# Kernel tuning notes

Hardware: AMD Instinct MI355X
Metric: run time of the kernel (lower is better)

The kernel has to match this reference:

```python
import jax, jax.numpy as jnp
import numpy as np

N, E, IN_DIM, OUT_DIM, HEADS = 50000, 800000, 128, 64, 2
NEG_SLOPE = 0.2  # DGL GATConv default leaky_relu slope


def setup_inputs() -> dict:
    key = jax.random.key(0)
    ks = jax.random.split(key, 11)
    p = lambda k, shape: jax.random.normal(k, shape, jnp.float32) * 0.05
    return dict(
        feature=jax.random.normal(ks[0], (N, IN_DIM), jnp.float32),
        src=jax.random.randint(ks[1], (E,), 0, N, jnp.int32),
        dst=jax.random.randint(ks[2], (E,), 0, N, jnp.int32),
        W1=p(ks[3], (IN_DIM, HEADS * OUT_DIM)),
        al1=p(ks[4], (HEADS, OUT_DIM)),
        ar1=p(ks[5], (HEADS, OUT_DIM)),
        b1=p(ks[6], (HEADS * OUT_DIM,)),
        W2=p(ks[7], (HEADS * OUT_DIM, OUT_DIM)),
        al2=p(ks[8], (1, OUT_DIM)),
        ar2=p(ks[9], (1, OUT_DIM)),
        b2=p(ks[10], (OUT_DIM,)),
    )


def gat_conv(x, W, al, ar, b, src, dst, n_nodes):
    # DGL GATConv (eval mode): fc -> per-node attn halves -> edge leaky_relu
    # -> edge-softmax grouped by dst -> scatter-weighted sum -> + bias
    H, D = al.shape
    h = (x @ W).reshape(n_nodes, H, D)               # [N,H,D]
    el = jnp.einsum('nhd,hd->nh', h, al)             # [N,H]
    er = jnp.einsum('nhd,hd->nh', h, ar)             # [N,H]
    e = jax.nn.leaky_relu(el[src] + er[dst], NEG_SLOPE)  # [E,H]
    m = jax.ops.segment_max(e, dst, num_segments=n_nodes)
    m = jnp.where(jnp.isfinite(m), m, 0.0)           # guard isolated dst nodes
    ex = jnp.exp(e - m[dst])                         # [E,H]
    s = jax.ops.segment_sum(ex, dst, num_segments=n_nodes)
    alpha = ex / s[dst]                              # edge-softmax weights
    out = jax.ops.segment_sum(alpha[:, :, None] * h[src], dst,
                              num_segments=n_nodes)  # [N,H,D]
    return out + b.reshape(H, D)


def reference(feature, src, dst, W1, al1, ar1, b1, W2, al2, ar2, b2):
    h1 = jax.nn.elu(gat_conv(feature, W1, al1, ar1, b1, src, dst, N))  # [N,2,D]
    h2 = gat_conv(h1.reshape(N, -1), W2, al2, ar2, b2, src, dst, N)    # [N,1,D]
    return (h1.mean(axis=1) + h2[:, 0, :]) * 0.5
```

## Files before the change

kernel.cpp:

```cpp
#include <hip/hip_runtime.h>
#include <hip/hip_fp16.h>
#include <math.h>

#define NNODES 50000
#define NEDGES 800000
#define CSR_STRIDE 48

typedef short bf16x8 __attribute__((ext_vector_type(8)));
typedef float f32x4  __attribute__((ext_vector_type(4)));

__device__ __forceinline__ unsigned bfpack(float a, float b) {
    unsigned ua = __float_as_uint(a), ub = __float_as_uint(b);
    ua = (ua + 0x7fffu + ((ua >> 16) & 1u)) >> 16;
    ub = (ub + 0x7fffu + ((ub >> 16) & 1u)) >> 16;
    return ua | (ub << 16);
}
__device__ __forceinline__ unsigned h2pack(float a, float b) {
    __half2 h = __floats2half2_rn(a, b);
    return *(unsigned*)&h;
}
__device__ __forceinline__ float hlo(unsigned u) {
    union { unsigned u; __half2 h; } c; c.u = u; return __half2float(c.h.x);
}
__device__ __forceinline__ float hhi(unsigned u) {
    union { unsigned u; __half2 h; } c; c.u = u; return __half2float(c.h.y);
}

__global__ __launch_bounds__(256) void fill_fused_kernel(
    const int* __restrict__ src, const int* __restrict__ dst,
    int* __restrict__ deg, unsigned short* __restrict__ pcsr) {
    const int t  = blockIdx.x * 256 + threadIdx.x;
    const int e0 = t * 4;
    if (e0 + 3 < NEDGES) {
        int4 d4 = *(const int4*)&dst[e0];
        int4 s4 = *(const int4*)&src[e0];
        int p0 = atomicAdd(&deg[d4.x], 1);
        int p1 = atomicAdd(&deg[d4.y], 1);
        int p2 = atomicAdd(&deg[d4.z], 1);
        int p3 = atomicAdd(&deg[d4.w], 1);
        if (p0 < CSR_STRIDE) pcsr[d4.x * CSR_STRIDE + p0] = (unsigned short)s4.x;
        if (p1 < CSR_STRIDE) pcsr[d4.y * CSR_STRIDE + p1] = (unsigned short)s4.y;
        if (p2 < CSR_STRIDE) pcsr[d4.z * CSR_STRIDE + p2] = (unsigned short)s4.z;
        if (p3 < CSR_STRIDE) pcsr[d4.w * CSR_STRIDE + p3] = (unsigned short)s4.w;
    } else if (e0 < NEDGES) {
        for (int e = e0; e < NEDGES; ++e) {
            int d = dst[e], s = src[e];
            int p = atomicAdd(&deg[d], 1);
            if (p < CSR_STRIDE) pcsr[d * CSR_STRIDE + p] = (unsigned short)s;
        }
    }
}

__global__ __launch_bounds__(256) void wt_kernel(const float* __restrict__ W1,
                                                 const float* __restrict__ W2,
                                                 unsigned* __restrict__ W1t,
                                                 unsigned* __restrict__ W2t) {
    int w = blockIdx.x * 256 + threadIdx.x;
    if (w < 8192) {
        int n = w >> 6, j = w & 63;
        W1t[w] = bfpack(W1[(2 * j) * 128 + n], W1[(2 * j + 1) * 128 + n]);
    } else {
        int w2 = w - 8192;
        int n = w2 >> 6, j = w2 & 63;
        W2t[w2] = bfpack(W2[(2 * j) * 64 + n], W2[(2 * j + 1) * 64 + n]);
    }
}

__global__ __launch_bounds__(256) void gemm1_kernel(
    const float* __restrict__ feat, const unsigned* __restrict__ Wt,
    const float* __restrict__ al, const float* __restrict__ ar,
    unsigned* __restrict__ h, float* __restrict__ el, float* __restrict__ er) {
    __shared__ unsigned Wb[128 * 68];
    __shared__ unsigned Ab[64 * 68];
    const int tid = threadIdx.x;
    const int n0  = blockIdx.x * 64;

#pragma unroll
    for (int i = 0; i < 8; ++i) {
        int id = i * 256 + tid;
        int n = id >> 4, c = (id & 15) * 4;
        *(uint4*)&Wb[n * 68 + c] = *(const uint4*)&Wt[n * 64 + c];
    }
#pragma unroll
    for (int i = 0; i < 8; ++i) {
        int f = i * 256 + tid;
        int m = f >> 5, cf = (f & 31) * 4;
        float4 v = make_float4(0.f, 0.f, 0.f, 0.f);
        if (n0 + m < NNODES)
            v = *(const float4*)&feat[(size_t)(n0 + m) * 128 + cf];
        uint2 p = {bfpack(v.x, v.y), bfpack(v.z, v.w)};
        *(uint2*)&Ab[m * 68 + cf / 2] = p;
    }
    __syncthreads();

    const int w  = tid >> 6;
    const int l  = tid & 63;
    const int ml = l & 15;
    const int q  = l >> 4;
    f32x4 acc[8];
#pragma unroll
    for (int t = 0; t < 8; ++t) acc[t] = (f32x4){0.f, 0.f, 0.f, 0.f};

#pragma unroll
    for (int kc = 0; kc < 4; ++kc) {
        const int kw = kc * 16 + q * 4;
        uint4 a4 = *(uint4*)&Ab[(16 * w + ml) * 68 + kw];
        bf16x8 af = *(bf16x8*)&a4;
#pragma unroll
        for (int t = 0; t < 8; ++t) {
            uint4 b4 = *(uint4*)&Wb[(t * 16 + ml) * 68 + kw];
            bf16x8 bf = *(bf16x8*)&b4;
            acc[t] = __builtin_amdgcn_mfma_f32_16x16x32_bf16(af, bf, acc[t], 0, 0, 0);
        }
    }

    float av[8], rv[8];
#pragma unroll
    for (int t = 0; t < 8; ++t) { av[t] = al[t * 16 + ml]; rv[t] = ar[t * 16 + ml]; }

#pragma unroll
    for (int r = 0; r < 4; ++r) {
        const int node = n0 + 16 * w + q * 4 + r;
        float e0 = 0.f, e1 = 0.f, f0 = 0.f, f1 = 0.f;
#pragma unroll
        for (int t = 0; t < 8; ++t) {
            float v = acc[t][r];
            if (t < 4) { e0 = fmaf(v, av[t], e0); f0 = fmaf(v, rv[t], f0); }
            else       { e1 = fmaf(v, av[t], e1); f1 = fmaf(v, rv[t], f1); }
            float pv = __shfl_xor(v, 1);
            if ((ml & 1) == 0 && node < NNODES)
                h[(size_t)node * 64 + t * 8 + (ml >> 1)] = h2pack(v, pv);
        }
#pragma unroll
        for (int mm = 1; mm <= 8; mm <<= 1) {
            e0 += __shfl_xor(e0, mm); e1 += __shfl_xor(e1, mm);
            f0 += __shfl_xor(f0, mm); f1 += __shfl_xor(f1, mm);
        }
        if (ml == 0 && node < NNODES) {
            el[node * 2 + 0] = e0; el[node * 2 + 1] = e1;
            er[node * 2 + 0] = f0; er[node * 2 + 1] = f1;
        }
    }
}

__global__ __launch_bounds__(256) void gemm2_kernel(
    const unsigned* __restrict__ h1b, const unsigned* __restrict__ Wt,
    const float* __restrict__ al, const float* __restrict__ ar,
    unsigned* __restrict__ h2, float* __restrict__ el, float* __restrict__ er) {
    __shared__ unsigned Wb[64 * 68];
    __shared__ unsigned Ab[64 * 68];
    const int tid = threadIdx.x;
    const int n0  = blockIdx.x * 64;

#pragma unroll
    for (int i = 0; i < 4; ++i) {
        int id = i * 256 + tid;
        int n = id >> 4, c = (id & 15) * 4;
        *(uint4*)&Wb[n * 68 + c] = *(const uint4*)&Wt[n * 64 + c];
    }
#pragma unroll
    for (int i = 0; i < 4; ++i) {
        int id = i * 256 + tid;
        int m = id >> 4, c = (id & 15) * 4;
        uint4 v = make_uint4(0u, 0u, 0u, 0u);
        if (n0 + m < NNODES)
            v = *(const uint4*)&h1b[(size_t)(n0 + m) * 64 + c];
        *(uint4*)&Ab[m * 68 + c] = v;
    }
    __syncthreads();

    const int w  = tid >> 6;
    const int l  = tid & 63;
    const int ml = l & 15;
    const int q  = l >> 4;
    f32x4 acc[4];
#pragma unroll
    for (int t = 0; t < 4; ++t) acc[t] = (f32x4){0.f, 0.f, 0.f, 0.f};

#pragma unroll
    for (int kc = 0; kc < 4; ++kc) {
        const int kw = kc * 16 + q * 4;
        uint4 a4 = *(uint4*)&Ab[(16 * w + ml) * 68 + kw];
        bf16x8 af = *(bf16x8*)&a4;
#pragma unroll
        for (int t = 0; t < 4; ++t) {
            uint4 b4 = *(uint4*)&Wb[(t * 16 + ml) * 68 + kw];
            bf16x8 bf = *(bf16x8*)&b4;
            acc[t] = __builtin_amdgcn_mfma_f32_16x16x32_bf16(af, bf, acc[t], 0, 0, 0);
        }
    }

    float av[4], rv[4];
#pragma unroll
    for (int t = 0; t < 4; ++t) { av[t] = al[t * 16 + ml]; rv[t] = ar[t * 16 + ml]; }

#pragma unroll
    for (int r = 0; r < 4; ++r) {
        const int node = n0 + 16 * w + q * 4 + r;
        float e0 = 0.f, f0 = 0.f;
#pragma unroll
        for (int t = 0; t < 4; ++t) {
            float v = acc[t][r];
            e0 = fmaf(v, av[t], e0);
            f0 = fmaf(v, rv[t], f0);
            float pv = __shfl_xor(v, 1);
            if ((ml & 1) == 0 && node < NNODES)
                h2[(size_t)node * 32 + t * 8 + (ml >> 1)] = h2pack(v, pv);
        }
#pragma unroll
        for (int mm = 1; mm <= 8; mm <<= 1) {
            e0 += __shfl_xor(e0, mm);
            f0 += __shfl_xor(f0, mm);
        }
        if (ml == 0 && node < NNODES) { el[node] = e0; er[node] = f0; }
    }
}

#define FMA8(hv, A)                                              \
    a0r = fmaf(hlo(hv.x), A, a0r); a1r = fmaf(hhi(hv.x), A, a1r); \
    a2r = fmaf(hlo(hv.y), A, a2r); a3r = fmaf(hhi(hv.y), A, a3r); \
    a4r = fmaf(hlo(hv.z), A, a4r); a5r = fmaf(hhi(hv.z), A, a5r); \
    a6r = fmaf(hlo(hv.w), A, a6r); a7r = fmaf(hhi(hv.w), A, a7r);

__global__ __launch_bounds__(256) void aggregate1_kernel(
    const int* __restrict__ degv,
    const unsigned short* __restrict__ csr_src,
    const float* __restrict__ el, const float* __restrict__ er,
    const unsigned* __restrict__ hh, const float* __restrict__ bias,
    unsigned* __restrict__ h1b, float* __restrict__ hm) {
    const int wid  = (blockIdx.x * 256 + threadIdx.x) >> 6;
    const int lane = threadIdx.x & 63;
    const int hl   = lane & 31;
    const int lb   = lane & 32;
    const int node = wid * 2 + (lane >> 5);
    if (node >= NNODES) return;
    const int row = node * CSR_STRIDE;
    int deg = degv[node];
    deg = deg < CSR_STRIDE ? deg : CSR_STRIDE;
    const float er0 = er[node * 2 + 0];
    const float er1 = er[node * 2 + 1];

    const int  q2    = hl >> 4;
    const int  ql    = hl & 15;
    const bool h1sel = (ql >= 8);
    const unsigned* __restrict__ hq = hh + 4 * ql;

    int s_reg = 0;
    if (hl < deg) s_reg = (int)csr_src[row + hl];

    uint4 hv[8];
#pragma unroll
    for (int j = 0; j < 8; ++j) {
        int s = __shfl(s_reg, lb + 2 * j + q2);
        hv[j] = *(const uint4*)(hq + (size_t)s * 64);
    }
    int dm  = deg < 32 ? deg : 32;
    int dmW = max(dm, __shfl_xor(dm, 32));
    const bool doB = dmW > 16;
    uint4 hw[8];
    if (doB) {
#pragma unroll
        for (int j = 0; j < 8; ++j) {
            int s = __shfl(s_reg, lb + 16 + 2 * j + q2);
            hw[j] = *(const uint4*)(hq + (size_t)s * 64);
        }
    }

    float2 e2 = *(const float2*)&el[s_reg * 2];
    float a = e2.x + er0; a = a > 0.f ? a : 0.2f * a;
    float b = e2.y + er1; b = b > 0.f ? b : 0.2f * b;
    float v0 = (hl < deg) ? a : -1e30f;
    float v1 = (hl < deg) ? b : -1e30f;
    float m0 = v0, m1 = v1;
    for (int i = 32 + hl; i < deg; i += 32) {
        int s = (int)csr_src[row + i];
        float2 ee = *(const float2*)&el[s * 2];
        float aa = ee.x + er0; aa = aa > 0.f ? aa : 0.2f * aa;
        float bb = ee.y + er1; bb = bb > 0.f ? bb : 0.2f * bb;
        m0 = fmaxf(m0, aa); m1 = fmaxf(m1, bb);
    }
#pragma unroll
    for (int off = 16; off > 0; off >>= 1) {
        m0 = fmaxf(m0, __shfl_xor(m0, off));
        m1 = fmaxf(m1, __shfl_xor(m1, off));
    }
    float p0 = __expf(v0 - m0);
    float p1 = __expf(v1 - m1);
    float ssum0 = p0, ssum1 = p1;
    for (int i = 32 + hl; i < deg; i += 32) {
        int s = (int)csr_src[row + i];
        float2 ee = *(const float2*)&el[s * 2];
        float aa = ee.x + er0; aa = aa > 0.f ? aa : 0.2f * aa;
        float bb = ee.y + er1; bb = bb > 0.f ? bb : 0.2f * bb;
        ssum0 += __expf(aa - m0); ssum1 += __expf(bb - m1);
    }
#pragma unroll
    for (int off = 16; off > 0; off >>= 1) {
        ssum0 += __shfl_xor(ssum0, off);
        ssum1 += __shfl_xor(ssum1, off);
    }

    float a0r = 0.f, a1r = 0.f, a2r = 0.f, a3r = 0.f;
    float a4r = 0.f, a5r = 0.f, a6r = 0.f, a7r = 0.f;
#pragma unroll
    for (int j = 0; j < 8; ++j) {
        const int sl_ = lb + 2 * j + q2;
        float x = __shfl(p0, sl_);
        float y = __shfl(p1, sl_);
        float A = h1sel ? y : x;
        FMA8(hv[j], A)
    }
    if (doB) {
#pragma unroll
        for (int j = 0; j < 8; ++j) {
            const int sl_ = lb + 16 + 2 * j + q2;
            float x = __shfl(p0, sl_);
            float y = __shfl(p1, sl_);
            float A = h1sel ? y : x;
            FMA8(hw[j], A)
        }
    }
    for (int i2 = 32; i2 < deg; i2 += 2) {
        int eidx = i2 + q2;
        if (eidx < deg) {
            int s = (int)csr_src[row + eidx];
            float2 ee = *(const float2*)&el[s * 2];
            float aa = ee.x + er0; aa = aa > 0.f ? aa : 0.2f * aa;
            float bb = ee.y + er1; bb = bb > 0.f ? bb : 0.2f * bb;
            float alpha = h1sel ? __expf(bb - m1) : __expf(aa - m0);
            uint4 h4 = *(const uint4*)(hq + (size_t)s * 64);
            FMA8(h4, alpha)
        }
    }
    a0r += __shfl_xor(a0r, 16);  a1r += __shfl_xor(a1r, 16);
    a2r += __shfl_xor(a2r, 16);  a3r += __shfl_xor(a3r, 16);
    a4r += __shfl_xor(a4r, 16);  a5r += __shfl_xor(a5r, 16);
    a6r += __shfl_xor(a6r, 16);  a7r += __shfl_xor(a7r, 16);

    const float ssum = h1sel ? ssum1 : ssum0;
    const float inv  = (deg > 0) ? 1.f / ssum : 0.f;
    float4 b0 = *(const float4*)&bias[8 * ql];
    float4 b1 = *(const float4*)&bias[8 * ql + 4];
    float o0 = fmaf(a0r, inv, b0.x), o1 = fmaf(a1r, inv, b0.y);
    float o2 = fmaf(a2r, inv, b0.z), o3 = fmaf(a3r, inv, b0.w);
    float o4 = fmaf(a4r, inv, b1.x), o5 = fmaf(a5r, inv, b1.y);
    float o6 = fmaf(a6r, inv, b1.z), o7 = fmaf(a7r, inv, b1.w);
    o0 = o0 > 0.f ? o0 : (__expf(o0) - 1.f);
    o1 = o1 > 0.f ? o1 : (__expf(o1) - 1.f);
    o2 = o2 > 0.f ? o2 : (__expf(o2) - 1.f);
    o3 = o3 > 0.f ? o3 : (__expf(o3) - 1.f);
    o4 = o4 > 0.f ? o4 : (__expf(o4) - 1.f);
    o5 = o5 > 0.f ? o5 : (__expf(o5) - 1.f);
    o6 = o6 > 0.f ? o6 : (__expf(o6) - 1.f);
    o7 = o7 > 0.f ? o7 : (__expf(o7) - 1.f);

    if (hl < 16) {
        uint4 pk;
        pk.x = bfpack(o0, o1); pk.y = bfpack(o2, o3);
        pk.z = bfpack(o4, o5); pk.w = bfpack(o6, o7);
        *(uint4*)&h1b[(size_t)node * 64 + 4 * ql] = pk;
    }
    float n0_ = 0.5f * (o0 + __shfl_xor(o0, 8));
    float n1_ = 0.5f * (o1 + __shfl_xor(o1, 8));
    float n2_ = 0.5f * (o2 + __shfl_xor(o2, 8));
    float n3_ = 0.5f * (o3 + __shfl_xor(o3, 8));
    float n4_ = 0.5f * (o4 + __shfl_xor(o4, 8));
    float n5_ = 0.5f * (o5 + __shfl_xor(o5, 8));
    float n6_ = 0.5f * (o6 + __shfl_xor(o6, 8));
    float n7_ = 0.5f * (o7 + __shfl_xor(o7, 8));
    if (hl < 8) {
        *(float4*)&hm[(size_t)node * 64 + 8 * hl]     = make_float4(n0_, n1_, n2_, n3_);
        *(float4*)&hm[(size_t)node * 64 + 8 * hl + 4] = make_float4(n4_, n5_, n6_, n7_);
    }
}

#define FMA4(hv, P)                                            \
    ax = fmaf(hlo(hv.x), P, ax); ay = fmaf(hhi(hv.x), P, ay);  \
    az = fmaf(hlo(hv.y), P, az); aw = fmaf(hhi(hv.y), P, aw);

__global__ __launch_bounds__(256) void aggregate2_kernel(
    const int* __restrict__ degv,
    const unsigned short* __restrict__ csr_src,
    const float* __restrict__ el, const float* __restrict__ er,
    const unsigned* __restrict__ hh, const float* __restrict__ bias,
    const float* __restrict__ hm, float* __restrict__ outp) {
    const int wid  = (blockIdx.x * 256 + threadIdx.x) >> 6;
    const int lane = threadIdx.x & 63;
    const int hl   = lane & 31;
    const int lb   = lane & 32;
    const int node = wid * 2 + (lane >> 5);
    if (node >= NNODES) return;
    const int row = node * CSR_STRIDE;
    int deg = degv[node];
    deg = deg < CSR_STRIDE ? deg : CSR_STRIDE;
    const float erd = er[node];

    const int s2 = hl >> 4;
    const int sl = hl & 15;
    const unsigned* __restrict__ hq = hh + 2 * sl;

    int s_reg = 0;
    if (hl < deg) s_reg = (int)csr_src[row + hl];

    uint2 hv[8];
#pragma unroll
    for (int j = 0; j < 8; ++j) {
        int s = __shfl(s_reg, lb + 2 * j + s2);
        hv[j] = *(const uint2*)(hq + (size_t)s * 32);
    }
    int dm  = deg < 32 ? deg : 32;
    int dmW = max(dm, __shfl_xor(dm, 32));
    const bool doB = dmW > 16;
    uint2 hw[8];
    if (doB) {
#pragma unroll
        for (int j = 0; j < 8; ++j) {
            int s = __shfl(s_reg, lb + 16 + 2 * j + s2);
            hw[j] = *(const uint2*)(hq + (size_t)s * 32);
        }
    }

    float v = el[s_reg] + erd;
    v = v > 0.f ? v : 0.2f * v;
    float v_reg = (hl < deg) ? v : -1e30f;
    float m = v_reg;
    for (int i = 32 + hl; i < deg; i += 32) {
        int s = (int)csr_src[row + i];
        float vv = el[s] + erd;
        vv = vv > 0.f ? vv : 0.2f * vv;
        m = fmaxf(m, vv);
    }
#pragma unroll
    for (int off = 16; off > 0; off >>= 1) m = fmaxf(m, __shfl_xor(m, off));

    float p_reg = __expf(v_reg - m);
    float ssum = p_reg;
    for (int i = 32 + hl; i < deg; i += 32) {
        int s = (int)csr_src[row + i];
        float vv = el[s] + erd;
        vv = vv > 0.f ? vv : 0.2f * vv;
        ssum += __expf(vv - m);
    }
#pragma unroll
    for (int off = 16; off > 0; off >>= 1) ssum += __shfl_xor(ssum, off);

    float ax = 0.f, ay = 0.f, az = 0.f, aw = 0.f;
#pragma unroll
    for (int j = 0; j < 8; ++j) {
        const int sl_ = lb + 2 * j + s2;
        float p = __shfl(p_reg, sl_);
        FMA4(hv[j], p)
    }
    if (doB) {
#pragma unroll
        for (int j = 0; j < 8; ++j) {
            const int sl_ = lb + 16 + 2 * j + s2;
            float p = __shfl(p_reg, sl_);
            FMA4(hw[j], p)
        }
    }
    for (int i2 = 32; i2 < deg; i2 += 2) {
        int eidx = i2 + s2;
        if (eidx < deg) {
            int s = (int)csr_src[row + eidx];
            float vv = el[s] + erd;
            vv = vv > 0.f ? vv : 0.2f * vv;
            float p = __expf(vv - m);
            uint2 h2v = *(const uint2*)(hq + (size_t)s * 32);
            FMA4(h2v, p)
        }
    }
    ax += __shfl_xor(ax, 16);  ay += __shfl_xor(ay, 16);
    az += __shfl_xor(az, 16);  aw += __shfl_xor(aw, 16);

    if (sl == hl) {
        float inv = (deg > 0) ? 1.f / ssum : 0.f;
        float4 hmv = *(const float4*)&hm[(size_t)node * 64 + 4 * sl];
        float4 bb  = *(const float4*)&bias[4 * sl];
        float o0 = (hmv.x + fmaf(ax, inv, bb.x)) * 0.5f;
        float o1 = (hmv.y + fmaf(ay, inv, bb.y)) * 0.5f;
        float o2 = (hmv.z + fmaf(az, inv, bb.z)) * 0.5f;
        float o3 = (hmv.w + fmaf(aw, inv, bb.w)) * 0.5f;
        *(float4*)&outp[(size_t)node * 64 + 4 * sl] = make_float4(o0, o1, o2, o3);
    }
}


extern "C" void kernel_launch(void* const* d_in, const int* in_sizes, int n_in,
                              void* d_out, int out_size, void* d_ws, size_t ws_size,
                              hipStream_t stream) {
    const float* feat = (const float*)d_in[0];
    const int*   src  = (const int*)d_in[1];
    const int*   dst  = (const int*)d_in[2];
    const float* W1   = (const float*)d_in[3];
    const float* al1  = (const float*)d_in[4];
    const float* ar1  = (const float*)d_in[5];
    const float* b1   = (const float*)d_in[6];
    const float* W2   = (const float*)d_in[7];
    const float* al2  = (const float*)d_in[8];
    const float* ar2  = (const float*)d_in[9];
    const float* b2   = (const float*)d_in[10];
    float* out = (float*)d_out;

    int*            ideg   = (int*)d_ws;
    unsigned*       iw1t   = (unsigned*)(ideg + NNODES);
    unsigned*       iw2t   = iw1t + 8192;
    unsigned short* pcsr   = (unsigned short*)(iw2t + 4096);
    unsigned*       gH1    = (unsigned*)(pcsr + (size_t)NNODES * CSR_STRIDE);
    unsigned*       gH2    = gH1;
    unsigned*       h1b    = gH1 + (size_t)NNODES * 64;
    float*          hmean  = (float*)(h1b + (size_t)NNODES * 64);
    float*          fEl1   = hmean + (size_t)NNODES * 64;
    float*          fEr1   = fEl1 + (size_t)NNODES * 2;
    float*          fEl2   = fEr1 + (size_t)NNODES * 2;
    float*          fEr2   = fEl2 + (size_t)NNODES;

    hipMemsetAsync(ideg, 0, NNODES * sizeof(int), stream);
    fill_fused_kernel<<<(NEDGES / 4 + 255) / 256, 256, 0, stream>>>(src, dst,
                                                                    ideg, pcsr);
    wt_kernel<<<48, 256, 0, stream>>>(W1, W2, iw1t, iw2t);

    gemm1_kernel<<<(NNODES + 63) / 64, 256, 0, stream>>>(feat, iw1t, al1, ar1,
                                                         gH1, fEl1, fEr1);
    aggregate1_kernel<<<(NNODES / 2 + 3) / 4, 256, 0, stream>>>(
        ideg, pcsr, fEl1, fEr1, gH1, b1, h1b, hmean);

    gemm2_kernel<<<(NNODES + 63) / 64, 256, 0, stream>>>(h1b, iw2t, al2, ar2,
                                                         gH2, fEl2, fEr2);
    aggregate2_kernel<<<(NNODES / 2 + 3) / 4, 256, 0, stream>>>(
        ideg, pcsr, fEl2, fEr2, gH2, b2, hmean, out);
}
```

Before: 229.3 us.

## Build padded CSR via two-pass bucket sort with shared-memory atomics

Replaces the single-pass global-atomic CSR fill with a two-stage bucketing scheme. The first kernel counts edges per 196-node bucket in LDS, reserves space with one global atomic per bucket, and scatters packed (local dst, src) words into bucket buffers. The second kernel builds each bucket's per-node degree and adjacency list in LDS and writes them out with coalesced vector stores. This is meant to remove the contention and scattered writes of 800k global atomics, at the cost of an extra pass over the edges and a fixed bucket capacity that silently drops edges if a bucket overflows.

New measurement: 207.3 us. -9.6%, faster.

```diff
diff --git a/kernel.cpp b/kernel.cpp
--- a/kernel.cpp
+++ b/kernel.cpp
@@ -5,6 +5,10 @@
 #define NNODES 50000
 #define NEDGES 800000
 #define CSR_STRIDE 48
+#define NBUCKET 256
+#define CHUNK 196
+#define BCAP 4096
+#define EPB 4096
 
 typedef short bf16x8 __attribute__((ext_vector_type(8)));
 typedef float f32x4  __attribute__((ext_vector_type(4)));
@@ -26,29 +30,57 @@
     union { unsigned u; __half2 h; } c; c.u = u; return __half2float(c.h.y);
 }
 
-__global__ __launch_bounds__(256) void fill_fused_kernel(
+__global__ __launch_bounds__(256) void bucketA_kernel(
     const int* __restrict__ src, const int* __restrict__ dst,
+    int* __restrict__ bcnt, unsigned* __restrict__ bbuf) {
+    __shared__ int lcnt[NBUCKET];
+    __shared__ int lcur[NBUCKET];
+    const int tid = threadIdx.x;
+    lcnt[tid] = 0;
+    __syncthreads();
+    const int e0 = blockIdx.x * EPB;
+    int e1 = e0 + EPB; if (e1 > NEDGES) e1 = NEDGES;
+    for (int e = e0 + tid; e < e1; e += 256)
+        atomicAdd(&lcnt[dst[e] / CHUNK], 1);
+    __syncthreads();
+    int c = lcnt[tid];
+    int base = 0;
+    if (c > 0) base = atomicAdd(&bcnt[tid], c);
+    lcur[tid] = tid * BCAP + base;
+    __syncthreads();
+    for (int e = e0 + tid; e < e1; e += 256) {
+        int d = dst[e], s = src[e];
+        int b = d / CHUNK;
+        int pos = atomicAdd(&lcur[b], 1);
+        if (pos < (b + 1) * BCAP)
+            bbuf[pos] = ((unsigned)(d - b * CHUNK) << 16) | (unsigned)s;
+    }
+}
+
+__global__ __launch_bounds__(256) void bucketB_kernel(
+    const int* __restrict__ bcnt, const unsigned* __restrict__ bbuf,
     int* __restrict__ deg, unsigned short* __restrict__ pcsr) {
-    const int t  = blockIdx.x * 256 + threadIdx.x;
-    const int e0 = t * 4;
-    if (e0 + 3 < NEDGES) {
-        int4 d4 = *(const int4*)&dst[e0];
-        int4 s4 = *(const int4*)&src[e0];
-        int p0 = atomicAdd(&deg[d4.x], 1);
-        int p1 = atomicAdd(&deg[d4.y], 1);
-        int p2 = atomicAdd(&deg[d4.z], 1);
-        int p3 = atomicAdd(&deg[d4.w], 1);
-        if (p0 < CSR_STRIDE) pcsr[d4.x * CSR_STRIDE + p0] = (unsigned short)s4.x;
-        if (p1 < CSR_STRIDE) pcsr[d4.y * CSR_STRIDE + p1] = (unsigned short)s4.y;
-        if (p2 < CSR_STRIDE) pcsr[d4.z * CSR_STRIDE + p2] = (unsigned short)s4.z;
-        if (p3 < CSR_STRIDE) pcsr[d4.w * CSR_STRIDE + p3] = (unsigned short)s4.w;
-    } else if (e0 < NEDGES) {
-        for (int e = e0; e < NEDGES; ++e) {
-            int d = dst[e], s = src[e];
-            int p = atomicAdd(&deg[d], 1);
-            if (p < CSR_STRIDE) pcsr[d * CSR_STRIDE + p] = (unsigned short)s;
-        }
-    }
+    const int b = blockIdx.x, tid = threadIdx.x;
+    const int n0 = b * CHUNK;
+    int ncnt = NNODES - n0; if (ncnt > CHUNK) ncnt = CHUNK;
+    __shared__ int ldeg[CHUNK];
+    __shared__ unsigned short lcsr[CHUNK * CSR_STRIDE];
+    for (int i = tid; i < CHUNK; i += 256) ldeg[i] = 0;
+    __syncthreads();
+    int cnt = bcnt[b]; if (cnt > BCAP) cnt = BCAP;
+    const unsigned* bb = bbuf + (size_t)b * BCAP;
+    for (int i = tid; i < cnt; i += 256) {
+        unsigned e = bb[i];
+        int ln = e >> 16;
+        int p = atomicAdd(&ldeg[ln], 1);
+        if (p < CSR_STRIDE) lcsr[ln * CSR_STRIDE + p] = (unsigned short)(e & 0xffffu);
+    }
+    __syncthreads();
+    for (int i = tid; i < ncnt; i += 256) deg[n0 + i] = ldeg[i];
+    const int nv = ncnt * (CSR_STRIDE / 8);
+    uint4* d4 = (uint4*)(pcsr + (size_t)n0 * CSR_STRIDE);
+    const uint4* s4 = (const uint4*)lcsr;
+    for (int i = tid; i < nv; i += 256) d4[i] = s4[i];
 }
 
 __global__ __launch_bounds__(256) void wt_kernel(const float* __restrict__ W1,
@@ -502,11 +534,13 @@
     const float* b2   = (const float*)d_in[10];
     float* out = (float*)d_out;
 
-    int*            ideg   = (int*)d_ws;
+    int*            bcnt   = (int*)d_ws;
+    int*            ideg   = bcnt + NBUCKET;
     unsigned*       iw1t   = (unsigned*)(ideg + NNODES);
     unsigned*       iw2t   = iw1t + 8192;
     unsigned short* pcsr   = (unsigned short*)(iw2t + 4096);
     unsigned*       gH1    = (unsigned*)(pcsr + (size_t)NNODES * CSR_STRIDE);
+    unsigned*       bbuf   = gH1;
     unsigned*       gH2    = gH1;
     unsigned*       h1b    = gH1 + (size_t)NNODES * 64;
     float*          hmean  = (float*)(h1b + (size_t)NNODES * 64);
@@ -515,9 +549,9 @@
     float*          fEl2   = fEr1 + (size_t)NNODES * 2;
     float*          fEr2   = fEl2 + (size_t)NNODES;
 
-    hipMemsetAsync(ideg, 0, NNODES * sizeof(int), stream);
-    fill_fused_kernel<<<(NEDGES / 4 + 255) / 256, 256, 0, stream>>>(src, dst,
-                                                                    ideg, pcsr);
+    hipMemsetAsync(bcnt, 0, NBUCKET * sizeof(int), stream);
+    bucketA_kernel<<<(NEDGES + EPB - 1) / EPB, 256, 0, stream>>>(src, dst, bcnt, bbuf);
+    bucketB_kernel<<<NBUCKET, 256, 0, stream>>>(bcnt, bbuf, ideg, pcsr);
     wt_kernel<<<48, 256, 0, stream>>>(W1, W2, iw1t, iw2t);
 
     gemm1_kernel<<<(NNODES + 63) / 64, 256, 0, stream>>>(feat, iw1t, al1, ar1,
```
